# Optimization experiments

Hardware: AMD Instinct MI355X
Metric: run time of the kernel (lower is better)

## Reference

```python
import jax, jax.numpy as jnp
import numpy as np

EMBED = 1024
HEADS = 16
HEAD_DIM = EMBED // HEADS
FF = 4 * EMBED
B, S = 2, 2048
EPS = 1e-5


def layer_norm(x, g, b):
    mu = jnp.mean(x, axis=-1, keepdims=True)
    var = jnp.mean(jnp.square(x - mu), axis=-1, keepdims=True)
    return (x - mu) * jax.lax.rsqrt(var + EPS) * g + b


def setup_inputs() -> dict:
    key = jax.random.key(0)
    ks = jax.random.split(key, 12)
    sc = 0.02
    x = jax.random.normal(ks[0], (B, S, EMBED), dtype=jnp.float32)
    # causal mask: 1 where attending allowed (mask==0 -> -inf in original)
    mask = jnp.tril(jnp.ones((S, S), dtype=jnp.int32))[None, None]
    return {
        "x": x,
        "mask": mask,
        "ln1_g": jnp.ones((EMBED,), jnp.float32),
        "ln1_b": jnp.zeros((EMBED,), jnp.float32),
        "wq": sc * jax.random.normal(ks[1], (EMBED, EMBED), jnp.float32),
        "bq": jnp.zeros((EMBED,), jnp.float32),
        "wk": sc * jax.random.normal(ks[2], (EMBED, EMBED), jnp.float32),
        "bk": jnp.zeros((EMBED,), jnp.float32),
        "wv": sc * jax.random.normal(ks[3], (EMBED, EMBED), jnp.float32),
        "bv": jnp.zeros((EMBED,), jnp.float32),
        "wo": sc * jax.random.normal(ks[4], (EMBED, EMBED), jnp.float32),
        "bo": jnp.zeros((EMBED,), jnp.float32),
        "ln2_g": jnp.ones((EMBED,), jnp.float32),
        "ln2_b": jnp.zeros((EMBED,), jnp.float32),
        "w1": sc * jax.random.normal(ks[5], (EMBED, FF), jnp.float32),
        "b1": jnp.zeros((FF,), jnp.float32),
        "w2": sc * jax.random.normal(ks[6], (FF, EMBED), jnp.float32),
        "b2": jnp.zeros((EMBED,), jnp.float32),
    }


def reference(x, mask, ln1_g, ln1_b, wq, bq, wk, bk, wv, bv, wo, bo,
              ln2_g, ln2_b, w1, b1, w2, b2):
    bsz, seq, _ = x.shape
    residual = x
    h = layer_norm(x, ln1_g, ln1_b)
    # QKV projections -> [B, H, S, Dh]
    def split_heads(t):
        return t.reshape(bsz, seq, HEADS, HEAD_DIM).transpose(0, 2, 1, 3)
    q = split_heads(h @ wq + bq)
    k = split_heads(h @ wk + bk)
    v = split_heads(h @ wv + bv)
    scores = jnp.einsum('bhqd,bhkd->bhqk', q, k) / (HEAD_DIM ** 0.5)
    scores = jnp.where(mask == 0, -jnp.inf, scores)
    attn = jax.nn.softmax(scores, axis=-1)
    out = jnp.einsum('bhqk,bhkd->bhqd', attn, v)
    out = out.transpose(0, 2, 1, 3).reshape(bsz, seq, EMBED)
    out = out @ wo + bo
    x = residual + out
    residual = x
    h = layer_norm(x, ln2_g, ln2_b)
    h = jax.nn.gelu(h @ w1 + b1, approximate=False) @ w2 + b2
    return residual + h
```

## Files before the change

### kernel.cpp

```cpp
#include <hip/hip_runtime.h>

typedef unsigned short u16;
typedef unsigned int   u32;
typedef __attribute__((ext_vector_type(8))) short bf16x8;
typedef __attribute__((ext_vector_type(4))) float f32x4;

#define S_LEN 2048
#define EMB   1024
#define NH    16
#define HD    64
#define FF_DIM 4096
#define NROWS 4096

__device__ __forceinline__ float b2f(u16 u){ union{u32 i; float f;} c; c.i = ((u32)u)<<16; return c.f; }
__device__ __forceinline__ u16 f2b(float f){ union{float f; u32 u;} c; c.f=f; return (u16)((c.u + 0x8000u)>>16); }
__device__ __forceinline__ float gelu_f(float x){
    float z  = x * 0.70710678118f;
    float az = fabsf(z);
    float t  = 1.0f / (1.0f + 0.3275911f * az);
    float p  = ((((1.061405429f*t - 1.453152027f)*t + 1.421413741f)*t - 0.284496736f)*t + 0.254829592f)*t;
    float e  = __expf(-az*az);
    float erfv = 1.0f - p*e;
    erfv = (z < 0.f) ? -erfv : erfv;
    return 0.5f*x*(1.0f + erfv);
}

__device__ __forceinline__ void load_lds16(const u16* g, u16* l) {
    __builtin_amdgcn_global_load_lds((const __attribute__((address_space(1))) u32*)g,
                                     (__attribute__((address_space(3))) u32*)l, 16, 0, 0);
}

template<int XF32>
__global__ __launch_bounds__(256)
void ln_kernel(const void* __restrict__ Xv, const float* __restrict__ G,
               const float* __restrict__ Bv, u16* __restrict__ Y)
{
    const int row = blockIdx.x, t = threadIdx.x;
    float v0, v1, v2, v3;
    if constexpr (XF32) {
        float4 r4 = ((const float4*)((const float*)Xv + (size_t)row*EMB))[t];
        v0 = r4.x; v1 = r4.y; v2 = r4.z; v3 = r4.w;
    } else {
        const u16* xr = (const u16*)Xv + (size_t)row*EMB;
        uint2 raw = *(const uint2*)(xr + t*4);
        v0 = b2f(raw.x & 0xffff); v1 = b2f(raw.x >> 16);
        v2 = b2f(raw.y & 0xffff); v3 = b2f(raw.y >> 16);
    }
    float s  = v0+v1+v2+v3;
    float s2 = v0*v0+v1*v1+v2*v2+v3*v3;
    #pragma unroll
    for (int off = 1; off < 64; off <<= 1) {
        s  += __shfl_xor(s,  off, 64);
        s2 += __shfl_xor(s2, off, 64);
    }
    __shared__ float ps[4], ps2[4];
    const int w = t >> 6, lane = t & 63;
    if (lane == 0) { ps[w] = s; ps2[w] = s2; }
    __syncthreads();
    s  = ps[0]+ps[1]+ps[2]+ps[3];
    s2 = ps2[0]+ps2[1]+ps2[2]+ps2[3];
    const float mu   = s * (1.0f/EMB);
    const float rstd = rsqrtf(fmaxf(s2*(1.0f/EMB) - mu*mu, 0.f) + 1e-5f);
    float4 g4 = ((const float4*)G)[t];
    float4 c4 = ((const float4*)Bv)[t];
    u32 lo = (u32)f2b((v0-mu)*rstd*g4.x + c4.x) | ((u32)f2b((v1-mu)*rstd*g4.y + c4.y) << 16);
    u32 hi = (u32)f2b((v2-mu)*rstd*g4.z + c4.z) | ((u32)f2b((v3-mu)*rstd*g4.w + c4.w) << 16);
    uint2 o; o.x = lo; o.y = hi;
    *(uint2*)(Y + (size_t)row*EMB + t*4) = o;
}

__global__ __launch_bounds__(256)
void transpose_k(const float* __restrict__ in, u16* __restrict__ out, int K, int N)
{
    __shared__ __align__(16) u16 T[64*72];
    const int k0 = blockIdx.y*64, n0 = blockIdx.x*64, t = threadIdx.x;
    #pragma unroll
    for (int c = 0; c < 4; ++c) {
        int e = t*4 + c*1024, ki = e >> 6, nj = e & 63;
        float4 f = *(const float4*)(in + (size_t)(k0+ki)*N + n0 + nj);
        ushort4 s4; s4.x = f2b(f.x); s4.y = f2b(f.y); s4.z = f2b(f.z); s4.w = f2b(f.w);
        *(ushort4*)&T[ki*72 + nj] = s4;
    }
    __syncthreads();
    #pragma unroll
    for (int c = 0; c < 2; ++c) {
        int e = t*8 + c*2048, ni = e >> 6, kj = e & 63;
        uint4 v; u16* pv = (u16*)&v;
        #pragma unroll
        for (int j = 0; j < 8; ++j) pv[j] = T[(kj+j)*72 + ni];
        *(uint4*)(out + (size_t)(n0+ni)*K + k0 + kj) = v;
    }
}

__global__ __launch_bounds__(256)
void vtrans(const u16* __restrict__ in, u16* __restrict__ out)
{
    __shared__ __align__(16) u16 T[64*72];
    const int bh = blockIdx.y, s0 = blockIdx.x*64, t = threadIdx.x;
    const size_t base = (size_t)bh * (S_LEN*HD);
    #pragma unroll
    for (int c = 0; c < 2; ++c) {
        int e = t*8 + c*2048, r = e >> 6, d = e & 63;
        *(uint4*)&T[r*72 + d] = *(const uint4*)(in + base + (size_t)(s0 + r)*HD + d);
    }
    __syncthreads();
    #pragma unroll
    for (int c = 0; c < 2; ++c) {
        int e = t*8 + c*2048, d = e >> 6, sj = e & 63;
        uint4 v; u16* pv = (u16*)&v;
        #pragma unroll
        for (int j = 0; j < 8; ++j) pv[j] = T[(sj + j)*72 + d];
        *(uint4*)(out + base + (size_t)d*S_LEN + s0 + sj) = v;
    }
}

__device__ __forceinline__ void stage2(const u16* s0, const u16* s1, int koff, u16* dst, int wave){
    load_lds16(s0 + koff, dst + wave*512);
    load_lds16(s1 + koff, dst + 4096 + wave*512);
}

template<int CBUF, int KS, int MFH, int TAILVM>
__device__ __forceinline__ void phase256(u16* Ls, f32x4 (&acc)[8][4], bf16x8 (&bf)[4],
    int wm, int wn, int lr, int quad, int wave,
    const u16* s0, const u16* s1, int koff, u16* dst)
{
    const u16* ak = Ls + CBUF*32768 + KS*8192;
    const u16* bk = Ls + CBUF*32768 + 16384 + KS*8192;
    bf16x8 af[4];
    #pragma unroll
    for (int i = 0; i < 4; ++i) {
        int off = (wm*128 + (MFH*4 + i)*16 + lr)*32 + quad*8;
        af[i] = *(const bf16x8*)(ak + (off ^ ((off>>3)&0x18)));
    }
    if constexpr (MFH == 0) {
        #pragma unroll
        for (int nf = 0; nf < 4; ++nf) {
            int off = (wn*64 + nf*16 + lr)*32 + quad*8;
            bf[nf] = *(const bf16x8*)(bk + (off ^ ((off>>3)&0x18)));
        }
    }
    stage2(s0, s1, koff, dst, wave);
    __builtin_amdgcn_s_barrier();
    asm volatile("s_waitcnt lgkmcnt(0)" ::: "memory");
    __builtin_amdgcn_s_setprio(1);
    #pragma unroll
    for (int i = 0; i < 4; ++i)
        #pragma unroll
        for (int nf = 0; nf < 4; ++nf)
            acc[MFH*4 + i][nf] = __builtin_amdgcn_mfma_f32_16x16x32_bf16(af[i], bf[nf], acc[MFH*4 + i][nf], 0, 0, 0);
    __builtin_amdgcn_s_setprio(0);
    if constexpr (TAILVM) asm volatile("s_waitcnt vmcnt(4)" ::: "memory");
    __builtin_amdgcn_s_barrier();
}

__device__ __forceinline__ void gemm256_main(u16* Ls, f32x4 (&acc)[8][4],
    int wm, int wn, int lr, int quad, int wave, int NT,
    const u16* srcA0, const u16* srcA1, const u16* srcB0, const u16* srcB1)
{
    u16* A00 = Ls + 0;
    u16* A01 = Ls + 8192;
    u16* B00 = Ls + 16384;
    u16* B01 = Ls + 16384 + 8192;
    u16* A10 = Ls + 32768;
    u16* A11 = Ls + 32768 + 8192;
    u16* B10 = Ls + 32768 + 16384;
    u16* B11 = Ls + 32768 + 16384 + 8192;

    stage2(srcA0, srcA1, 0,   A00, wave);
    stage2(srcB0, srcB1, 0,   B00, wave);
    stage2(srcA0, srcA1, 32,  A01, wave);
    stage2(srcB0, srcB1, 32,  B01, wave);
    stage2(srcA0, srcA1, 64,  A10, wave);
    stage2(srcB0, srcB1, 64,  B10, wave);
    asm volatile("s_waitcnt vmcnt(4)" ::: "memory");
    __builtin_amdgcn_s_barrier();

    bf16x8 bf[4];
    for (int U = 0; U < NT; U += 2) {
        const int k1 = ((U+1) & (NT-1))*64;
        const int k2 = ((U+2) & (NT-1))*64;
        const int k3 = ((U+3) & (NT-1))*64;
        phase256<0,0,0,0>(Ls, acc, bf, wm, wn, lr, quad, wave, srcA0, srcA1, k1+32, A11);
        phase256<0,0,1,0>(Ls, acc, bf, wm, wn, lr, quad, wave, srcB0, srcB1, k1+32, B11);
        phase256<0,1,0,0>(Ls, acc, bf, wm, wn, lr, quad, wave, srcA0, srcA1, k2,    A00);
        phase256<0,1,1,1>(Ls, acc, bf, wm, wn, lr, quad, wave, srcB0, srcB1, k2,    B00);
        phase256<1,0,0,0>(Ls, acc, bf, wm, wn, lr, quad, wave, srcA0, srcA1, k2+32, A01);
        phase256<1,0,1,0>(Ls, acc, bf, wm, wn, lr, quad, wave, srcB0, srcB1, k2+32, B01);
        phase256<1,1,0,0>(Ls, acc, bf, wm, wn, lr, quad, wave, srcA0, srcA1, k3,    A10);
        phase256<1,1,1,1>(Ls, acc, bf, wm, wn, lr, quad, wave, srcB0, srcB1, k3,    B10);
    }

    asm volatile("s_waitcnt vmcnt(0)" ::: "memory");
    __syncthreads();
}

template<int MODE>
__global__ __launch_bounds__(512, 2)
void gemm256(const u16* __restrict__ A, const u16* __restrict__ Bt,
             const float* __restrict__ bias, const float* __restrict__ bias2,
             const float* __restrict__ bias3,
             void* __restrict__ C, void* __restrict__ C2, void* __restrict__ C3,
             int M, int N, int K)
{
    (void)M;
    __shared__ __align__(16) u16 Ls[65536];
    const int t = threadIdx.x;
    const int wave = t >> 6, lane = t & 63;
    const int wm = wave >> 2, wn = wave & 3;
    const int lr = lane & 15, quad = lane >> 4;
    const int n0 = blockIdx.x*256, m0 = blockIdx.y*256;

    const int c0 = wave*64 + lane, c1 = 512 + wave*64 + lane;
    const int l0 = c0 ^ ((c0 >> 3) & 3), l1 = c1 ^ ((c1 >> 3) & 3);
    const int r0 = l0 >> 2, g0 = l0 & 3;
    const int r1 = l1 >> 2, g1 = l1 & 3;
    const u16* srcA0 = A  + (size_t)(m0 + r0)*K + g0*8;
    const u16* srcA1 = A  + (size_t)(m0 + r1)*K + g1*8;
    const u16* srcB0 = Bt + (size_t)(n0 + r0)*K + g0*8;
    const u16* srcB1 = Bt + (size_t)(n0 + r1)*K + g1*8;

    f32x4 acc[8][4];
    const f32x4 fzero = {0.f, 0.f, 0.f, 0.f};
    #pragma unroll
    for (int i = 0; i < 8; ++i)
        #pragma unroll
        for (int j = 0; j < 4; ++j) acc[i][j] = fzero;

    gemm256_main(Ls, acc, wm, wn, lr, quad, wave, K >> 6, srcA0, srcA1, srcB0, srcB1);

    float bv[4];
    #pragma unroll
    for (int nf = 0; nf < 4; ++nf) {
        const int col = n0 + wn*64 + nf*16 + lr;
        if constexpr (MODE == 5) {
            const int seg = n0 >> 10;
            bv[nf] = (seg == 0 ? bias : (seg == 1 ? bias2 : bias3))[col & 1023];
        } else {
            bv[nf] = bias[col];
        }
    }
    #pragma unroll
    for (int mf = 0; mf < 8; ++mf)
        #pragma unroll
        for (int nf = 0; nf < 4; ++nf)
            #pragma unroll
            for (int r = 0; r < 4; ++r) {
                float v = acc[mf][nf][r] + bv[nf];
                if constexpr (MODE == 2) v = gelu_f(v);
                Ls[(wm*128 + mf*16 + quad*4 + r)*256 + wn*64 + nf*16 + lr] = f2b(v);
            }
    __syncthreads();
    #pragma unroll
    for (int j = 0; j < 16; ++j) {
        const int idx = j*512 + t;
        const int rr = idx >> 5, ck = idx & 31;
        const u16* src = Ls + rr*256 + ck*8;
        const int row = m0 + rr, col = n0 + ck*8;
        if constexpr (MODE == 5) {
            const int seg = n0 >> 10;
            u16* dstb = (u16*)(seg == 0 ? C : (seg == 1 ? C2 : C3));
            const int cs = col & 1023;
            const int h = cs >> 6, d = cs & 63;
            const int b_ = row >> 11, s = row & 2047;
            *(uint4*)(dstb + ((((size_t)(b_*NH + h))*S_LEN + s) << 6) + d) = *(const uint4*)src;
        } else {
            *(uint4*)((u16*)C + (size_t)row*N + col) = *(const uint4*)src;
        }
    }
}

__global__ __launch_bounds__(512, 2)
void gemm256sk(const u16* __restrict__ A, const u16* __restrict__ Bt,
               u16* __restrict__ Cl, u16* __restrict__ Ch, int N, int K)
{
    __shared__ __align__(16) u16 Ls[65536];
    const int t = threadIdx.x;
    const int wave = t >> 6, lane = t & 63;
    const int wm = wave >> 2, wn = wave & 3;
    const int lr = lane & 15, quad = lane >> 4;
    const int n0 = blockIdx.x*256, m0 = blockIdx.y*256;
    const int z  = blockIdx.z;
    const int Ks = K >> 2;

    const int c0 = wave*64 + lane, c1 = 512 + wave*64 + lane;
    const int l0 = c0 ^ ((c0 >> 3) & 3), l1 = c1 ^ ((c1 >> 3) & 3);
    const int r0 = l0 >> 2, g0 = l0 & 3;
    const int r1 = l1 >> 2, g1 = l1 & 3;
    const u16* srcA0 = A  + (size_t)(m0 + r0)*K + g0*8 + z*Ks;
    const u16* srcA1 = A  + (size_t)(m0 + r1)*K + g1*8 + z*Ks;
    const u16* srcB0 = Bt + (size_t)(n0 + r0)*K + g0*8 + z*Ks;
    const u16* srcB1 = Bt + (size_t)(n0 + r1)*K + g1*8 + z*Ks;

    f32x4 acc[8][4];
    const f32x4 fzero = {0.f, 0.f, 0.f, 0.f};
    #pragma unroll
    for (int i = 0; i < 8; ++i)
        #pragma unroll
        for (int j = 0; j < 4; ++j) acc[i][j] = fzero;

    gemm256_main(Ls, acc, wm, wn, lr, quad, wave, Ks >> 6, srcA0, srcA1, srcB0, srcB1);

    #pragma unroll
    for (int mf = 0; mf < 8; ++mf)
        #pragma unroll
        for (int nf = 0; nf < 4; ++nf)
            #pragma unroll
            for (int r = 0; r < 4; ++r)
                Ls[(wm*128 + mf*16 + quad*4 + r)*256 + wn*64 + nf*16 + lr] = f2b(acc[mf][nf][r]);
    __syncthreads();
    u16* dst = (z < 2 ? Cl : Ch) + (size_t)(z & 1)*(1u<<22);
    #pragma unroll
    for (int j = 0; j < 16; ++j) {
        const int idx = j*512 + t;
        const int rr = idx >> 5, ck = idx & 31;
        *(uint4*)(dst + (size_t)(m0 + rr)*N + n0 + ck*8) = *(const uint4*)(Ls + rr*256 + ck*8);
    }
}

__global__ __launch_bounds__(256)
void reduce_wo(const u16* __restrict__ pl, const u16* __restrict__ ph,
               const float* __restrict__ xres, const float* __restrict__ bias,
               u16* __restrict__ y)
{
    const int i0 = (blockIdx.x*256 + threadIdx.x)*8;
    uint4 a0 = *(const uint4*)(pl + i0);
    uint4 a1 = *(const uint4*)(pl + (1u<<22) + i0);
    uint4 a2 = *(const uint4*)(ph + i0);
    uint4 a3 = *(const uint4*)(ph + (1u<<22) + i0);
    const int col = i0 & 1023;
    float4 b0 = *(const float4*)(bias + col);
    float4 b1 = *(const float4*)(bias + col + 4);
    float4 x0 = *(const float4*)(xres + i0);
    float4 x1 = *(const float4*)(xres + i0 + 4);
    const u16 *s0=(const u16*)&a0, *s1=(const u16*)&a1, *s2=(const u16*)&a2, *s3=(const u16*)&a3;
    const float bb[8] = {b0.x,b0.y,b0.z,b0.w,b1.x,b1.y,b1.z,b1.w};
    const float xx[8] = {x0.x,x0.y,x0.z,x0.w,x1.x,x1.y,x1.z,x1.w};
    u16 out[8];
    #pragma unroll
    for (int j = 0; j < 8; ++j)
        out[j] = f2b(b2f(s0[j]) + b2f(s1[j]) + b2f(s2[j]) + b2f(s3[j]) + bb[j] + xx[j]);
    *(uint4*)(y + i0) = *(const uint4*)out;
}

__global__ __launch_bounds__(256)
void reduce_ff2(const u16* __restrict__ pl, const u16* __restrict__ ph,
                const u16* __restrict__ x1b, const float* __restrict__ bias,
                float* __restrict__ out)
{
    const int i0 = (blockIdx.x*256 + threadIdx.x)*8;
    uint4 a0 = *(const uint4*)(pl + i0);
    uint4 a1 = *(const uint4*)(pl + (1u<<22) + i0);
    uint4 a2 = *(const uint4*)(ph + i0);
    uint4 a3 = *(const uint4*)(ph + (1u<<22) + i0);
    uint4 xr = *(const uint4*)(x1b + i0);
    const int col = i0 & 1023;
    float4 b0 = *(const float4*)(bias + col);
    float4 b1 = *(const float4*)(bias + col + 4);
    const u16 *s0=(const u16*)&a0, *s1=(const u16*)&a1, *s2=(const u16*)&a2, *s3=(const u16*)&a3;
    const u16 *xp=(const u16*)&xr;
    const float bb[8] = {b0.x,b0.y,b0.z,b0.w,b1.x,b1.y,b1.z,b1.w};
    float f[8];
    #pragma unroll
    for (int j = 0; j < 8; ++j)
        f[j] = b2f(s0[j]) + b2f(s1[j]) + b2f(s2[j]) + b2f(s3[j]) + b2f(xp[j]) + bb[j];
    float4 o0 = {f[0],f[1],f[2],f[3]}, o1 = {f[4],f[5],f[6],f[7]};
    *(float4*)(out + i0) = o0;
    *(float4*)(out + i0 + 4) = o1;
}

__global__ __launch_bounds__(256, 2)
void attn_kernel(const u16* __restrict__ Q, const u16* __restrict__ Kg,
                 const u16* __restrict__ Vt, u16* __restrict__ O)
{
    const int bh = blockIdx.x;
    const int pr = blockIdx.y;
    const int qta = pr, qtb = 31 - pr;
    const int t = threadIdx.x, wave = t >> 6, lane = t & 63;
    const int lr = lane & 15, quad = lane >> 4;

    __shared__ __align__(16) u16 Ks[4096];
    __shared__ __align__(16) u16 Vs[4096];
    __shared__ __align__(16) u16 Ps[4][16*72];

    const size_t qkbase = (size_t)bh * (S_LEN*HD);
    const int b = bh >> 4, h = bh & 15;
    u16* Pw = Ps[wave];
    const f32x4 fzero = {0.f, 0.f, 0.f, 0.f};

    const u16* qpa = Q + qkbase + (size_t)(qta*64 + wave*16 + lr)*HD + quad*8;
    const u16* qpb = Q + qkbase + (size_t)(qtb*64 + wave*16 + lr)*HD + quad*8;
    bf16x8 qa0 = *(const bf16x8*)qpa, qa1 = *(const bf16x8*)(qpa + 32);
    bf16x8 qb0 = *(const bf16x8*)qpb, qb1 = *(const bf16x8*)(qpb + 32);

    f32x4 oa[4], ob[4];
    float la[4], lb[4];
    #pragma unroll
    for (int dt = 0; dt < 4; ++dt) { oa[dt] = fzero; ob[dt] = fzero; }
    #pragma unroll
    for (int r = 0; r < 4; ++r) { la[r] = 0.f; lb[r] = 0.f; }

    const u16* gK = Kg + qkbase + (size_t)(wave*16 + (lane>>2))*HD + (lane&3)*8;
    const u16* gV = Vt + qkbase + (size_t)(wave*16 + (lane>>2))*S_LEN + (lane&3)*8;
    u16* lK = Ks + wave*512;
    u16* lV = Vs + wave*512;

    const int qrow_qa = qta*64 + wave*16 + quad*4;
    const int qrow_qb = qtb*64 + wave*16 + quad*4;

    for (int kb = 0; kb <= qtb; ++kb) {
        __syncthreads();
        load_lds16(gK + (size_t)kb*4096,      lK);
        load_lds16(gK + (size_t)kb*4096 + 32, lK + 2048);
        load_lds16(gV + kb*64,                lV);
        load_lds16(gV + kb*64 + 32,           lV + 2048);
        __syncthreads();

        #pragma unroll
        for (int tile = 0; tile < 2; ++tile) {
            const int qt = tile ? qta : qtb;
            if (tile && kb > qta) break;
            bf16x8 qf0 = tile ? qa0 : qb0;
            bf16x8 qf1 = tile ? qa1 : qb1;
            f32x4* oacc = tile ? oa : ob;
            float* lp   = tile ? la : lb;
            const int qrowq = tile ? qrow_qa : qrow_qb;

            f32x4 sc[4];
            #pragma unroll
            for (int kt2 = 0; kt2 < 4; ++kt2) {
                bf16x8 kf0 = *(const bf16x8*)&Ks[(kt2*16 + lr)*32 + quad*8];
                bf16x8 kf1 = *(const bf16x8*)&Ks[2048 + (kt2*16 + lr)*32 + quad*8];
                sc[kt2] = __builtin_amdgcn_mfma_f32_16x16x32_bf16(qf0, kf0, fzero, 0, 0, 0);
                sc[kt2] = __builtin_amdgcn_mfma_f32_16x16x32_bf16(qf1, kf1, sc[kt2], 0, 0, 0);
            }
            const bool diag = (kb == qt);
            #pragma unroll
            for (int r = 0; r < 4; ++r) {
                #pragma unroll
                for (int kt2 = 0; kt2 < 4; ++kt2) {
                    int kcol = kb*64 + kt2*16 + lr;
                    float p = (!diag || kcol <= qrowq + r) ? __expf(fminf(sc[kt2][r]*0.125f, 30.f)) : 0.f;
                    lp[r] += p;
                    Pw[(quad*4 + r)*72 + kt2*16 + lr] = f2b(p);
                }
            }
            bf16x8 pf0 = *(const bf16x8*)&Pw[lr*72 + quad*8];
            bf16x8 pf1 = *(const bf16x8*)&Pw[lr*72 + 32 + quad*8];
            #pragma unroll
            for (int dt = 0; dt < 4; ++dt) {
                bf16x8 vf0 = *(const bf16x8*)&Vs[(dt*16 + lr)*32 + quad*8];
                bf16x8 vf1 = *(const bf16x8*)&Vs[2048 + (dt*16 + lr)*32 + quad*8];
                oacc[dt] = __builtin_amdgcn_mfma_f32_16x16x32_bf16(pf0, vf0, oacc[dt], 0, 0, 0);
                oacc[dt] = __builtin_amdgcn_mfma_f32_16x16x32_bf16(pf1, vf1, oacc[dt], 0, 0, 0);
            }
        }
    }

    #pragma unroll
    for (int tile = 0; tile < 2; ++tile) {
        const int qt = tile ? qta : qtb;
        f32x4* oacc = tile ? oa : ob;
        float* lp   = tile ? la : lb;
        #pragma unroll
        for (int r = 0; r < 4; ++r) {
            float v = lp[r];
            v += __shfl_xor(v, 1, 64); v += __shfl_xor(v, 2, 64);
            v += __shfl_xor(v, 4, 64); v += __shfl_xor(v, 8, 64);
            lp[r] = 1.0f / fmaxf(v, 1e-20f);
        }
        #pragma unroll
        for (int dt = 0; dt < 4; ++dt)
            #pragma unroll
            for (int r = 0; r < 4; ++r)
                Pw[(quad*4 + r)*64 + dt*16 + lr] = f2b(oacc[dt][r] * lp[r]);

        const int q = lane >> 2, d0 = (lane & 3)*16;
        u16* dst = O + ((size_t)(b*S_LEN + qt*64 + wave*16 + q))*EMB + h*HD + d0;
        *(uint4*)(dst)     = *(uint4*)&Pw[q*64 + d0];
        *(uint4*)(dst + 8) = *(uint4*)&Pw[q*64 + d0 + 8];
    }
}

extern "C" void kernel_launch(void* const* d_in, const int* in_sizes, int n_in,
                              void* d_out, int out_size, void* d_ws, size_t ws_size,
                              hipStream_t stream)
{
    (void)in_sizes; (void)n_in; (void)out_size; (void)ws_size;
    const float* x    = (const float*)d_in[0];
    const float* ln1g = (const float*)d_in[2];
    const float* ln1b = (const float*)d_in[3];
    const float* wq = (const float*)d_in[4];  const float* bq = (const float*)d_in[5];
    const float* wk = (const float*)d_in[6];  const float* bk = (const float*)d_in[7];
    const float* wv = (const float*)d_in[8];  const float* bv = (const float*)d_in[9];
    const float* wo = (const float*)d_in[10]; const float* bo = (const float*)d_in[11];
    const float* ln2g = (const float*)d_in[12]; const float* ln2b = (const float*)d_in[13];
    const float* w1 = (const float*)d_in[14]; const float* b1 = (const float*)d_in[15];
    const float* w2 = (const float*)d_in[16]; const float* b2 = (const float*)d_in[17];

    u16* ws = (u16*)d_ws;
    const size_t M1 = 1u << 20;
    u16* wqkvT = ws + 0*M1;
    u16* wqT = ws + 0*M1;
    u16* wkT = ws + 1*M1;
    u16* wvT = ws + 2*M1;
    u16* woT = ws + 3*M1;
    u16* w2T = ws + 0*M1;
    u16* w1T = ws + 4*M1;
    u16* h0  = ws + 8*M1;
    u16* qb  = ws + 12*M1;
    u16* kb  = ws + 16*M1;
    u16* vT  = ws + 20*M1;
    u16* ao  = ws + 24*M1;
    u16* vb  = ws + 24*M1;
    u16* x1  = ws + 28*M1;
    u16* fb  = ws + 12*M1;
    u16* wosl = ws + 8*M1;
    u16* ffsl_lo = ws + 4*M1;
    u16* ffsl_hi = ws + 20*M1;

    dim3 blk(256);
    transpose_k<<<dim3(16,16), blk, 0, stream>>>(wq, wqT, EMB, EMB);
    transpose_k<<<dim3(16,16), blk, 0, stream>>>(wk, wkT, EMB, EMB);
    transpose_k<<<dim3(16,16), blk, 0, stream>>>(wv, wvT, EMB, EMB);
    transpose_k<<<dim3(16,16), blk, 0, stream>>>(wo, woT, EMB, EMB);
    transpose_k<<<dim3(64,16), blk, 0, stream>>>(w1, w1T, EMB, FF_DIM);

    ln_kernel<1><<<NROWS, blk, 0, stream>>>(x, ln1g, ln1b, h0);

    gemm256<5><<<dim3(12,16), dim3(512), 0, stream>>>(h0, wqkvT, bq, bk, bv,
                                                      qb, kb, vb, NROWS, 3072, EMB);

    vtrans<<<dim3(32,32), blk, 0, stream>>>(vb, vT);

    attn_kernel<<<dim3(32,16), blk, 0, stream>>>(qb, kb, vT, ao);

    gemm256sk<<<dim3(4,16,4), dim3(512), 0, stream>>>(ao, woT, wosl, wosl + 8*M1, EMB, EMB);
    reduce_wo<<<2048, blk, 0, stream>>>(wosl, wosl + 8*M1, x, bo, x1);

    transpose_k<<<dim3(16,64), blk, 0, stream>>>(w2, w2T, FF_DIM, EMB);

    ln_kernel<0><<<NROWS, blk, 0, stream>>>(x1, ln2g, ln2b, h0);

    gemm256<2><<<dim3(16,16), dim3(512), 0, stream>>>(h0, w1T, b1, nullptr, nullptr,
                                                      fb, nullptr, nullptr, NROWS, FF_DIM, EMB);

    gemm256sk<<<dim3(4,16,4), dim3(512), 0, stream>>>(fb, w2T, ffsl_lo, ffsl_hi, EMB, FF_DIM);
    reduce_ff2<<<2048, blk, 0, stream>>>(ffsl_lo, ffsl_hi, x1, b2, (float*)d_out);
}
```

Before: 364.4 us.

## Prefetch LDS fragments one phase ahead in 256-tile GEMM main loop

Restructures the GEMM main loop so the LDS reads for the next MFMA phase are issued before the current phase's MFMAs, using double sets of A/B fragment registers. The explicit lgkmcnt(0) wait before each MFMA block is removed and the compiler handles LDS read dependencies instead. This is meant to hide LDS latency behind matrix math. It raises register pressure, which under the launch_bounds of 2 blocks per CU could cause spills.

Result: no change. 363.7 us (-0.2%).

```diff
diff --git a/kernel.cpp b/kernel.cpp
--- a/kernel.cpp
+++ b/kernel.cpp
@@ -119,38 +119,32 @@
     load_lds16(s1 + koff, dst + 4096 + wave*512);
 }
 
-template<int CBUF, int KS, int MFH, int TAILVM>
-__device__ __forceinline__ void phase256(u16* Ls, f32x4 (&acc)[8][4], bf16x8 (&bf)[4],
-    int wm, int wn, int lr, int quad, int wave,
-    const u16* s0, const u16* s1, int koff, u16* dst)
-{
+template<int CBUF,int KS,int H>
+__device__ __forceinline__ void rdA4(const u16* Ls, int wm, int lr, int quad, bf16x8 (&d)[4]){
     const u16* ak = Ls + CBUF*32768 + KS*8192;
+    #pragma unroll
+    for (int i = 0; i < 4; ++i){
+        int off = (wm*128 + H*64 + i*16 + lr)*32 + quad*8;
+        d[i] = *(const bf16x8*)(ak + (off ^ ((off>>3)&0x18)));
+    }
+}
+template<int CBUF,int KS>
+__device__ __forceinline__ void rdB4(const u16* Ls, int wn, int lr, int quad, bf16x8 (&d)[4]){
     const u16* bk = Ls + CBUF*32768 + 16384 + KS*8192;
-    bf16x8 af[4];
-    #pragma unroll
-    for (int i = 0; i < 4; ++i) {
-        int off = (wm*128 + (MFH*4 + i)*16 + lr)*32 + quad*8;
-        af[i] = *(const bf16x8*)(ak + (off ^ ((off>>3)&0x18)));
-    }
-    if constexpr (MFH == 0) {
-        #pragma unroll
-        for (int nf = 0; nf < 4; ++nf) {
-            int off = (wn*64 + nf*16 + lr)*32 + quad*8;
-            bf[nf] = *(const bf16x8*)(bk + (off ^ ((off>>3)&0x18)));
-        }
-    }
-    stage2(s0, s1, koff, dst, wave);
-    __builtin_amdgcn_s_barrier();
-    asm volatile("s_waitcnt lgkmcnt(0)" ::: "memory");
+    #pragma unroll
+    for (int nf = 0; nf < 4; ++nf){
+        int off = (wn*64 + nf*16 + lr)*32 + quad*8;
+        d[nf] = *(const bf16x8*)(bk + (off ^ ((off>>3)&0x18)));
+    }
+}
+__device__ __forceinline__ void mm4(f32x4 (&acc)[8][4], int m0, const bf16x8 (&a)[4], const bf16x8 (&b)[4]){
     __builtin_amdgcn_s_setprio(1);
     #pragma unroll
     for (int i = 0; i < 4; ++i)
         #pragma unroll
         for (int nf = 0; nf < 4; ++nf)
-            acc[MFH*4 + i][nf] = __builtin_amdgcn_mfma_f32_16x16x32_bf16(af[i], bf[nf], acc[MFH*4 + i][nf], 0, 0, 0);
+            acc[m0+i][nf] = __builtin_amdgcn_mfma_f32_16x16x32_bf16(a[i], b[nf], acc[m0+i][nf], 0, 0, 0);
     __builtin_amdgcn_s_setprio(0);
-    if constexpr (TAILVM) asm volatile("s_waitcnt vmcnt(4)" ::: "memory");
-    __builtin_amdgcn_s_barrier();
 }
 
 __device__ __forceinline__ void gemm256_main(u16* Ls, f32x4 (&acc)[8][4],
@@ -175,19 +169,58 @@
     asm volatile("s_waitcnt vmcnt(4)" ::: "memory");
     __builtin_amdgcn_s_barrier();
 
-    bf16x8 bf[4];
+    bf16x8 aL0[4], aH0[4], bC0[4];
+    bf16x8 aL1[4], aH1[4], bC1[4];
     for (int U = 0; U < NT; U += 2) {
         const int k1 = ((U+1) & (NT-1))*64;
         const int k2 = ((U+2) & (NT-1))*64;
         const int k3 = ((U+3) & (NT-1))*64;
-        phase256<0,0,0,0>(Ls, acc, bf, wm, wn, lr, quad, wave, srcA0, srcA1, k1+32, A11);
-        phase256<0,0,1,0>(Ls, acc, bf, wm, wn, lr, quad, wave, srcB0, srcB1, k1+32, B11);
-        phase256<0,1,0,0>(Ls, acc, bf, wm, wn, lr, quad, wave, srcA0, srcA1, k2,    A00);
-        phase256<0,1,1,1>(Ls, acc, bf, wm, wn, lr, quad, wave, srcB0, srcB1, k2,    B00);
-        phase256<1,0,0,0>(Ls, acc, bf, wm, wn, lr, quad, wave, srcA0, srcA1, k2+32, A01);
-        phase256<1,0,1,0>(Ls, acc, bf, wm, wn, lr, quad, wave, srcB0, srcB1, k2+32, B01);
-        phase256<1,1,0,0>(Ls, acc, bf, wm, wn, lr, quad, wave, srcA0, srcA1, k3,    A10);
-        phase256<1,1,1,1>(Ls, acc, bf, wm, wn, lr, quad, wave, srcB0, srcB1, k3,    B10);
+        rdA4<0,0,0>(Ls, wm, lr, quad, aL0);
+        rdB4<0,0>  (Ls, wn, lr, quad, bC0);
+        rdA4<0,0,1>(Ls, wm, lr, quad, aH0);
+        stage2(srcA0, srcA1, k1+32, A11, wave);
+        __builtin_amdgcn_s_barrier();
+        mm4(acc, 0, aL0, bC0);
+        __builtin_amdgcn_s_barrier();
+        rdA4<0,1,0>(Ls, wm, lr, quad, aL1);
+        rdB4<0,1>  (Ls, wn, lr, quad, bC1);
+        stage2(srcB0, srcB1, k1+32, B11, wave);
+        __builtin_amdgcn_s_barrier();
+        mm4(acc, 4, aH0, bC0);
+        __builtin_amdgcn_s_barrier();
+        rdA4<0,1,1>(Ls, wm, lr, quad, aH1);
+        stage2(srcA0, srcA1, k2, A00, wave);
+        __builtin_amdgcn_s_barrier();
+        mm4(acc, 0, aL1, bC1);
+        __builtin_amdgcn_s_barrier();
+        stage2(srcB0, srcB1, k2, B00, wave);
+        __builtin_amdgcn_s_barrier();
+        mm4(acc, 4, aH1, bC1);
+        asm volatile("s_waitcnt vmcnt(4)" ::: "memory");
+        __builtin_amdgcn_s_barrier();
+        rdA4<1,0,0>(Ls, wm, lr, quad, aL0);
+        rdB4<1,0>  (Ls, wn, lr, quad, bC0);
+        rdA4<1,0,1>(Ls, wm, lr, quad, aH0);
+        stage2(srcA0, srcA1, k2+32, A01, wave);
+        __builtin_amdgcn_s_barrier();
+        mm4(acc, 0, aL0, bC0);
+        __builtin_amdgcn_s_barrier();
+        rdA4<1,1,0>(Ls, wm, lr, quad, aL1);
+        rdB4<1,1>  (Ls, wn, lr, quad, bC1);
+        stage2(srcB0, srcB1, k2+32, B01, wave);
+        __builtin_amdgcn_s_barrier();
+        mm4(acc, 4, aH0, bC0);
+        __builtin_amdgcn_s_barrier();
+        rdA4<1,1,1>(Ls, wm, lr, quad, aH1);
+        stage2(srcA0, srcA1, k3, A10, wave);
+        __builtin_amdgcn_s_barrier();
+        mm4(acc, 0, aL1, bC1);
+        __builtin_amdgcn_s_barrier();
+        stage2(srcB0, srcB1, k3, B10, wave);
+        __builtin_amdgcn_s_barrier();
+        mm4(acc, 4, aH1, bC1);
+        asm volatile("s_waitcnt vmcnt(4)" ::: "memory");
+        __builtin_amdgcn_s_barrier();
     }
 
     asm volatile("s_waitcnt vmcnt(0)" ::: "memory");
```
